# Kernel tuning notes

Hardware: AMD Instinct MI355X
Metric: run time of the kernel (lower is better)

Reference implementation:

```python
import jax, jax.numpy as jnp
import numpy as np
import math

B, T, HID = 2, 2048, 2048
NH, KH, HD = 32, 8, 64
G = NH // KH  # query heads per kv head
EPS = 1e-6
BASE = 10000.0


def _rope_sin_cos(t_len):
    inv_freq = 1.0 / (BASE ** (jnp.arange(0, HD, 2, dtype=jnp.float32) / HD))  # [HD/2]
    t = jnp.arange(t_len, dtype=jnp.float32)
    freqs = t[:, None] * inv_freq[None, :]  # [T, HD/2]
    return jnp.sin(freqs), jnp.cos(freqs)


def _apply_rope(x, sin, cos):
    # x: [B,H,T,D], pairwise interleaved rotation
    b, h, t, d = x.shape
    xr = x.reshape(b, h, t, d // 2, 2)
    x1, x2 = xr[..., 0], xr[..., 1]
    rot1 = x1 * cos - x2 * sin
    rot2 = x1 * sin + x2 * cos
    return jnp.stack((rot1, rot2), axis=-1).reshape(b, h, t, d)


def _rmsnorm(x, w):
    var = jnp.mean(x * x, axis=-1, keepdims=True)
    return x * jax.lax.rsqrt(var + EPS) * w


def setup_inputs() -> dict:
    key = jax.random.key(0)
    ks = jax.random.split(key, 5)
    s = 0.02
    return {
        "hidden_states": jax.random.normal(ks[0], (B, T, HID), jnp.float32),
        "wq": jax.random.normal(ks[1], (HID, HID), jnp.float32) * s,
        "wk": jax.random.normal(ks[2], (HID, KH * HD), jnp.float32) * s,
        "wv": jax.random.normal(ks[3], (HID, KH * HD), jnp.float32) * s,
        "wo": jax.random.normal(ks[4], (HID, HID), jnp.float32) * s,
        "q_norm_w": jnp.ones((HD,), jnp.float32),
        "k_norm_w": jnp.ones((HD,), jnp.float32),
    }


def reference(hidden_states, wq, wk, wv, wo, q_norm_w, k_norm_w):
    b, t, _ = hidden_states.shape
    # fused-ish QKV projections
    q = (hidden_states @ wq).reshape(b, t, NH, HD).transpose(0, 2, 1, 3)   # [B,NH,T,D]
    k = (hidden_states @ wk).reshape(b, t, KH, HD).transpose(0, 2, 1, 3)   # [B,KH,T,D]
    v = (hidden_states @ wv).reshape(b, t, KH, HD).transpose(0, 2, 1, 3)   # [B,KH,T,D]

    sin, cos = _rope_sin_cos(t)  # [T, D/2]
    q = _rmsnorm(_apply_rope(q, sin, cos), q_norm_w)
    k = _rmsnorm(_apply_rope(k, sin, cos), k_norm_w)

    scale = 1.0 / math.sqrt(HD)
    # grouped attention without materializing repeated KV
    qg = q.reshape(b, KH, G, t, HD)
    scores = jnp.einsum('bkgqd,bkld->bkgql', qg, k) * scale  # [B,KH,G,Tq,Tk]

    qi = jax.lax.broadcasted_iota(jnp.int32, (t, t), 0)
    ki = jax.lax.broadcasted_iota(jnp.int32, (t, t), 1)
    causal = ki <= qi
    scores = jnp.where(causal, scores, jnp.float32(-jnp.inf))

    attn = jax.nn.softmax(scores, axis=-1)
    ctx = jnp.einsum('bkgql,bkld->bkgqd', attn, v)  # [B,KH,G,T,D]
    ctx = ctx.reshape(b, NH, t, HD).transpose(0, 2, 1, 3).reshape(b, t, NH * HD)
    return ctx @ wo
```

## Files before the change

### kernel.cpp

```cpp
#include <hip/hip_runtime.h>
#include <math.h>
#include <stdint.h>

#define B_   2
#define T_   2048
#define HID_ 2048
#define NH_  32
#define KH_  8
#define HD_  64
#define LDQKV 3072

typedef unsigned short u16;
typedef __attribute__((ext_vector_type(8))) short v8s;
typedef __attribute__((ext_vector_type(4))) float v4f;

__device__ inline v4f mfma16(v8s a, v8s b, v4f c) {
    return __builtin_amdgcn_mfma_f32_16x16x32_bf16(a, b, c, 0, 0, 0);
}
__device__ inline u16 f2bf(float f) {
    uint32_t u = __float_as_uint(f);
    u += 0x7fff + ((u >> 16) & 1);
    return (u16)(u >> 16);
}
__device__ inline float bf2f(u16 h) { return __uint_as_float(((uint32_t)h) << 16); }
__device__ inline uint32_t cvtpk_bf16(float lo, float hi) {
    uint32_t r;
    asm("v_cvt_pk_bf16_f32 %0, %1, %2" : "=v"(r) : "v"(lo), "v"(hi));
    return r;
}

#define GLDS(g, s)                                                                     \
    __builtin_amdgcn_global_load_lds(                                                  \
        (const __attribute__((address_space(1))) uint32_t*)(uintptr_t)(g),             \
        (__attribute__((address_space(3))) uint32_t*)(uint32_t)(uintptr_t)(s), 16, 0, 0)

__global__ __launch_bounds__(256) void conv_f32_bf16(const float* __restrict__ in,
                                                     u16* __restrict__ out, int n4) {
    int i = blockIdx.x * 256 + threadIdx.x;
    if (i >= n4) return;
    float4 v = ((const float4*)in)[i];
    ushort4 o = {f2bf(v.x), f2bf(v.y), f2bf(v.z), f2bf(v.w)};
    ((ushort4*)out)[i] = o;
}

__global__ __launch_bounds__(256) void trconv4(const float* __restrict__ s0,
                                               const float* __restrict__ s1,
                                               const float* __restrict__ s2,
                                               const float* __restrict__ s3,
                                               u16* __restrict__ d0, u16* __restrict__ d1,
                                               u16* __restrict__ d2, u16* __restrict__ d3) {
    const int z = blockIdx.z;
    const float* in = (z == 0) ? s0 : (z == 1) ? s1 : (z == 2) ? s2 : s3;
    u16* out = (z == 0) ? d0 : (z == 1) ? d1 : (z == 2) ? d2 : d3;
    const int R = 2048;
    const int C = (z == 1 || z == 2) ? 512 : 2048;
    const int r0 = blockIdx.y * 64, c0 = blockIdx.x * 64;
    if (c0 >= C) return;

    __shared__ float t[64][65];
    const int tid = threadIdx.x;
#pragma unroll
    for (int i = 0; i < 16; ++i) {
        int idx = i * 256 + tid, r = idx >> 6, c = idx & 63;
        t[r][c] = in[(size_t)(r0 + r) * C + c0 + c];
    }
    __syncthreads();
#pragma unroll
    for (int i = 0; i < 16; ++i) {
        int idx = i * 256 + tid, r = idx >> 6, c = idx & 63;
        out[(size_t)(c0 + r) * R + r0 + c] = f2bf(t[c][r]);
    }
}

__global__ __launch_bounds__(256) void rope_table(float2* __restrict__ tab) {
    int i = blockIdx.x * 256 + threadIdx.x;
    int t = i >> 5, p = i & 31;
    float fr = (float)t * exp2f((float)p * (-13.28771237954945f / 32.0f));
    float2 sc; sc.x = sinf(fr); sc.y = cosf(fr);
    tab[i] = sc;
}

__global__ __launch_bounds__(256) void vtrans(const u16* __restrict__ V, u16* __restrict__ Vt) {
    const int t0 = blockIdx.x * 64, kh = blockIdx.y, b = blockIdx.z;
    const int tid = threadIdx.x;
    __shared__ __align__(16) u16 tl[64][72];
#pragma unroll
    for (int p = 0; p < 2; ++p) {
        int c = p * 256 + tid, trow = c >> 3, d8 = (c & 7) * 8;
        *(v8s*)&tl[trow][d8] =
            *(const v8s*)(V + (size_t)(b * T_ + t0 + trow) * LDQKV + kh * HD_ + d8);
    }
    __syncthreads();
#pragma unroll
    for (int p = 0; p < 2; ++p) {
        int c = p * 256 + tid, drow = c >> 3, t8 = (c & 7) * 8;
        v8s o;
#pragma unroll
        for (int j = 0; j < 8; ++j) o[j] = (short)tl[t8 + j][drow];
        *(v8s*)(Vt + ((size_t)((b * KH_ + kh) * HD_) + drow) * T_ + t0 + t8) = o;
    }
}

template <bool OBF>
__global__ __launch_bounds__(256) void gemm_mfma(const u16* __restrict__ A,
                                                 const u16* __restrict__ Bt,
                                                 void* __restrict__ Cv,
                                                 int M, int N, int K) {
    __shared__ __align__(16) u16 Al[128 * 32];
    __shared__ __align__(16) u16 Bl[128 * 32];
    const int tid = threadIdx.x;
    const int l = tid & 63;
    const int wid = tid >> 6;
    const int wr = wid >> 1, wc = wid & 1;
    const int lr = l & 15, lg = l >> 4;

    const int nx = gridDim.x;
    const int nwg = nx * gridDim.y;
    const int id = blockIdx.y * nx + blockIdx.x;
    const int sw = (id & 7) * (nwg >> 3) + (id >> 3);
    const int row0 = (sw / nx) * 128, col0 = (sw % nx) * 128;

    v4f acc[4][4];
    const v4f Z4 = {0.f, 0.f, 0.f, 0.f};
#pragma unroll
    for (int i = 0; i < 4; ++i)
#pragma unroll
        for (int j = 0; j < 4; ++j) acc[i][j] = Z4;

    const int m0 = tid & 127;
    const int ch0 = tid >> 7, ch1 = (256 + tid) >> 7;
    const u16* ga0 = A + (size_t)(row0 + m0) * K + ch0 * 8;
    const u16* ga1 = A + (size_t)(row0 + m0) * K + ch1 * 8;
    const u16* gb0 = Bt + (size_t)(col0 + m0) * K + ch0 * 8;
    const u16* gb1 = Bt + (size_t)(col0 + m0) * K + ch1 * 8;
    const int wbase = __builtin_amdgcn_readfirstlane(tid & 192);
    u16* la0 = &Al[wbase * 8];
    u16* la1 = &Al[(256 + wbase) * 8];
    u16* lb0 = &Bl[wbase * 8];
    u16* lb1 = &Bl[(256 + wbase) * 8];

    for (int k0 = 0; k0 < K; k0 += 32) {
        __syncthreads();
        GLDS(ga0 + k0, la0);
        GLDS(ga1 + k0, la1);
        GLDS(gb0 + k0, lb0);
        GLDS(gb1 + k0, lb1);
        __syncthreads();
        v8s af[4], bfr[4];
#pragma unroll
        for (int i = 0; i < 4; ++i) {
            af[i]  = *(const v8s*)&Al[(lg * 128 + wr * 64 + i * 16 + lr) * 8];
            bfr[i] = *(const v8s*)&Bl[(lg * 128 + wc * 64 + i * 16 + lr) * 8];
        }
#pragma unroll
        for (int i = 0; i < 4; ++i)
#pragma unroll
            for (int j = 0; j < 4; ++j) acc[i][j] = mfma16(af[i], bfr[j], acc[i][j]);
    }

#pragma unroll
    for (int i = 0; i < 4; ++i)
#pragma unroll
        for (int j = 0; j < 4; ++j)
#pragma unroll
            for (int r = 0; r < 4; ++r) {
                int row = row0 + wr * 64 + i * 16 + lg * 4 + r;
                int col = col0 + wc * 64 + j * 16 + lr;
                float v = acc[i][j][r];
                if (OBF) ((u16*)Cv)[(size_t)row * N + col] = f2bf(v);
                else     ((float*)Cv)[(size_t)row * N + col] = v;
            }
}

__global__ __launch_bounds__(256) void rope_rms2(u16* __restrict__ X,
                                                 const float* __restrict__ qw,
                                                 const float* __restrict__ kw,
                                                 const float2* __restrict__ tab) {
    int pair = blockIdx.x * 4 + (threadIdx.x >> 6);
    const int lane = threadIdx.x & 63;
    int row, h, off;
    const float* w;
    if (pair < 4096 * 32) { row = pair >> 5; h = pair & 31; off = 0; w = qw; }
    else { pair -= 4096 * 32; row = pair >> 3; h = pair & 7; off = 2048; w = kw; }
    const int t = row & (T_ - 1);

    u16* px = X + (size_t)row * LDQKV + off + h * HD_ + lane;
    float x = bf2f(*px);
    float2 sc = tab[t * 32 + (lane >> 1)];
    float other = __shfl_xor(x, 1, 64);
    float r = (lane & 1) ? fmaf(other, sc.x, x * sc.y) : fmaf(x, sc.y, -(other * sc.x));
    float sq = r * r;
#pragma unroll
    for (int offv = 32; offv >= 1; offv >>= 1) sq += __shfl_xor(sq, offv, 64);
    float invn = rsqrtf(sq * (1.0f / 64.0f) + 1e-6f);
    *px = f2bf(r * invn * w[lane]);
}

__global__ __launch_bounds__(512, 2) void attn_mfma(const u16* __restrict__ Qb,
                                                    const u16* __restrict__ Kb,
                                                    const u16* __restrict__ VTb,
                                                    u16* __restrict__ Ctx) {
    const int qt = gridDim.x - 1 - blockIdx.x;
    const int kh = blockIdx.y, b = blockIdx.z;
    const int tid = threadIdx.x, w = tid >> 6, l = tid & 63;
    const int lr = l & 15, lg = l >> 4;

    __shared__ __align__(16) u16 Kbuf[2][128 * 64];
    __shared__ __align__(16) u16 Vbuf[2][64 * 128];
    __shared__ __align__(16) uint32_t Ps[8][16][68];

    v8s qf[4][2];
#pragma unroll
    for (int g = 0; g < 4; ++g) {
        const u16* qp = Qb + (size_t)(b * T_ + qt * 128 + w * 16 + lr) * LDQKV +
                        (kh * 4 + g) * HD_ + lg * 8;
        qf[g][0] = *(const v8s*)qp;
        qf[g][1] = *(const v8s*)(qp + 32);
    }

    const int u0 = tid, u1 = 512 + tid;
    const int kr0 = u0 >> 3, kc0 = (u0 & 7) ^ (kr0 & 7);
    const int kr1 = u1 >> 3, kc1 = (u1 & 7) ^ (kr1 & 7);
    const u16* kg0 = Kb + (size_t)(b * T_ + kr0) * LDQKV + kh * HD_ + kc0 * 8;
    const u16* kg1 = Kb + (size_t)(b * T_ + kr1) * LDQKV + kh * HD_ + kc1 * 8;
    const int vr0 = u0 >> 4, vc0 = (u0 & 15) ^ (vr0 & 15);
    const int vr1 = u1 >> 4, vc1 = (u1 & 15) ^ (vr1 & 15);
    const u16* vg0 = VTb + ((size_t)((b * KH_ + kh) * HD_) + vr0) * T_ + vc0 * 8;
    const u16* vg1 = VTb + ((size_t)((b * KH_ + kh) * HD_) + vr1) * T_ + vc1 * 8;
    const int wu64 = __builtin_amdgcn_readfirstlane(w * 64);

    const v4f Z4 = {0.f, 0.f, 0.f, 0.f};
    v4f o[4][4];
    float lsum[4];
#pragma unroll
    for (int g = 0; g < 4; ++g) {
        lsum[g] = 0.f;
#pragma unroll
        for (int d = 0; d < 4; ++d) o[g][d] = Z4;
    }

    auto stage = [&](int bufi, int kt) {
        const size_t ko = (size_t)kt * 128 * LDQKV;
        const int vo = kt * 128;
        GLDS(kg0 + ko, &Kbuf[bufi][wu64 * 8]);
        GLDS(kg1 + ko, &Kbuf[bufi][(512 + wu64) * 8]);
        GLDS(vg0 + vo, &Vbuf[bufi][wu64 * 8]);
        GLDS(vg1 + vo, &Vbuf[bufi][(512 + wu64) * 8]);
    };

    const float C1 = 0.18033688011112042f;
    const float C0 = -11.541560327111707f;
    const int swz8 = lr & 7;

    auto body = [&](const u16* Kc, const u16* Vc, bool masked) {
#pragma unroll
        for (int g = 0; g < 4; ++g) {
            v4f s[8];
#pragma unroll
            for (int j = 0; j < 8; ++j) s[j] = Z4;
#pragma unroll
            for (int ks = 0; ks < 2; ++ks) {
#pragma unroll
                for (int j = 0; j < 8; ++j)
                    s[j] = mfma16(*(const v8s*)&Kc[(j * 16 + lr) * 64 + (((ks * 4 + lg) ^ swz8) * 8)],
                                  qf[g][ks], s[j]);
            }
#pragma unroll
            for (int j = 0; j < 8; ++j) {
                float p[4];
#pragma unroll
                for (int r = 0; r < 4; ++r) {
                    float pv = exp2f(fmaf(s[j][r], C1, C0));
                    if (masked && (j * 16 + lg * 4 + r) > (w * 16 + lr)) pv = 0.f;
                    p[r] = pv;
                }
                lsum[g] += (p[0] + p[1]) + (p[2] + p[3]);
                Ps[w][lr][j * 8 + lg * 2 + 0] = cvtpk_bf16(p[0], p[1]);
                Ps[w][lr][j * 8 + lg * 2 + 1] = cvtpk_bf16(p[2], p[3]);
            }
            asm volatile("s_waitcnt lgkmcnt(0)" ::: "memory");
#pragma unroll
            for (int ks = 0; ks < 4; ++ks) {
                v8s pf = *(const v8s*)&Ps[w][lr][ks * 16 + lg * 4];
#pragma unroll
                for (int dj = 0; dj < 4; ++dj)
                    o[g][dj] = mfma16(*(const v8s*)&Vc[(dj * 16 + lr) * 128 + (((ks * 4 + lg) ^ lr) * 8)],
                                      pf, o[g][dj]);
            }
        }
    };

    stage(0, 0);
    int buf = 0;
    for (int kt = 0; kt < qt; ++kt) {
        stage(buf ^ 1, kt + 1);
        asm volatile("s_waitcnt vmcnt(4)" ::: "memory");
        __builtin_amdgcn_s_barrier();
        body(Kbuf[buf], Vbuf[buf], false);
        asm volatile("s_waitcnt lgkmcnt(0)" ::: "memory");
        __builtin_amdgcn_s_barrier();
        buf ^= 1;
    }
    asm volatile("s_waitcnt vmcnt(0)" ::: "memory");
    __builtin_amdgcn_s_barrier();
    body(Kbuf[buf], Vbuf[buf], true);

#pragma unroll
    for (int g = 0; g < 4; ++g) {
        float t1 = lsum[g] + __shfl_xor(lsum[g], 16, 64);
        float inv = 1.0f / (t1 + __shfl_xor(t1, 32, 64));
        u16* cp = Ctx + (size_t)(b * T_ + qt * 128 + w * 16 + lr) * (NH_ * HD_) +
                  (kh * 4 + g) * HD_ + lg * 4;
#pragma unroll
        for (int dj = 0; dj < 4; ++dj) {
            ushort4 ov = {f2bf(o[g][dj][0] * inv), f2bf(o[g][dj][1] * inv),
                          f2bf(o[g][dj][2] * inv), f2bf(o[g][dj][3] * inv)};
            *(ushort4*)(cp + dj * 16) = ov;
        }
    }
}

extern "C" void kernel_launch(void* const* d_in, const int* in_sizes, int n_in,
                              void* d_out, int out_size, void* d_ws, size_t ws_size,
                              hipStream_t stream) {
    const float* hs  = (const float*)d_in[0];
    const float* wq  = (const float*)d_in[1];
    const float* wk  = (const float*)d_in[2];
    const float* wv  = (const float*)d_in[3];
    const float* wo  = (const float*)d_in[4];
    const float* qnw = (const float*)d_in[5];
    const float* knw = (const float*)d_in[6];
    float* out = (float*)d_out;
    (void)in_sizes; (void)n_in; (void)out_size; (void)ws_size;

    char* p = (char*)d_ws;
    auto alloc = [&](size_t bytes) { void* r = (void*)p; p += (bytes + 255) & ~(size_t)255; return r; };
    u16* hsb   = (u16*)alloc((size_t)4096 * 2048 * 2);
    u16* wqkvt = (u16*)alloc((size_t)3072 * 2048 * 2);
    u16* qkvb  = (u16*)alloc((size_t)4096 * 3072 * 2);
    u16* wot   = (u16*)alloc((size_t)2048 * 2048 * 2);
    u16* ctx   = (u16*)alloc((size_t)4096 * 2048 * 2);
    u16* vt    = (u16*)alloc((size_t)B_ * KH_ * HD_ * T_ * 2);
    float2* tab = (float2*)alloc((size_t)T_ * 32 * sizeof(float2));

    conv_f32_bf16<<<(4096 * 2048 / 4 + 255) / 256, 256, 0, stream>>>(hs, hsb, 4096 * 2048 / 4);
    trconv4<<<dim3(32, 32, 4), 256, 0, stream>>>(wq, wk, wv, wo,
                                                 wqkvt,
                                                 wqkvt + (size_t)2048 * 2048,
                                                 wqkvt + (size_t)2560 * 2048,
                                                 wot);
    rope_table<<<(T_ * 32) / 256, 256, 0, stream>>>(tab);

    gemm_mfma<true><<<dim3(3072 / 128, 4096 / 128), 256, 0, stream>>>(hsb, wqkvt, qkvb, 4096, 3072, 2048);

    rope_rms2<<<(4096 * 40) / 4, 256, 0, stream>>>(qkvb, qnw, knw, tab);
    vtrans<<<dim3(T_ / 64, KH_, B_), 256, 0, stream>>>(qkvb + 2560, vt);

    attn_mfma<<<dim3(T_ / 128, KH_, B_), 512, 0, stream>>>(qkvb, qkvb + 2048, vt, ctx);

    gemm_mfma<false><<<dim3(2048 / 128, 4096 / 128), 256, 0, stream>>>(ctx, wot, out, 4096, 2048, 2048);
}
```

Baseline: 440.7 us.

## Replace GEMM with double-buffered 256-row tile kernel using swizzled LDS and ping-pong

Replaces the simple single-buffered 128x128 MFMA GEMM with a 512-thread kernel that uses 256xBN tiles, a K-step of 64 split into two halves, and double-buffered LDS. Global-to-LDS loads for later tiles are issued while MFMAs on the current tile run, with explicit vmcnt waits, barriers and setprio to interleave memory and compute. LDS addresses are XOR-swizzled to avoid bank conflicts. It uses larger register and LDS footprints and hand-placed waitcnt counts, and it is applied to both the QKV and output projections.

```diff
diff --git a/kernel.cpp b/kernel.cpp
--- a/kernel.cpp
+++ b/kernel.cpp
@@ -33,6 +33,10 @@
     __builtin_amdgcn_global_load_lds(                                                  \
         (const __attribute__((address_space(1))) uint32_t*)(uintptr_t)(g),             \
         (__attribute__((address_space(3))) uint32_t*)(uint32_t)(uintptr_t)(s), 16, 0, 0)
+
+#define BAR() __builtin_amdgcn_s_barrier()
+#define LG0() asm volatile("s_waitcnt lgkmcnt(0)" ::: "memory")
+#define VMW(n) asm volatile("s_waitcnt vmcnt(" #n ")" ::: "memory")
 
 __global__ __launch_bounds__(256) void conv_f32_bf16(const float* __restrict__ in,
                                                      u16* __restrict__ out, int n4) {
@@ -101,75 +105,129 @@
     }
 }
 
-template <bool OBF>
-__global__ __launch_bounds__(256) void gemm_mfma(const u16* __restrict__ A,
-                                                 const u16* __restrict__ Bt,
-                                                 void* __restrict__ Cv,
-                                                 int M, int N, int K) {
-    __shared__ __align__(16) u16 Al[128 * 32];
-    __shared__ __align__(16) u16 Bl[128 * 32];
+template <int BN, bool OBF>
+__global__ __launch_bounds__(512, 2) void gemm8(const u16* __restrict__ A,
+                                                const u16* __restrict__ Bt,
+                                                void* __restrict__ Cv,
+                                                int M, int N, int K) {
+    constexpr int NW_N = BN / 64;
+    constexpr int MF = (NW_N == 4) ? 8 : 4;
+    constexpr int MH = MF / 2;
+
+    __shared__ __align__(16) u16 Al[2][2][8192];
+    __shared__ __align__(16) u16 Bl[2][2][BN * 32];
+
     const int tid = threadIdx.x;
-    const int l = tid & 63;
-    const int wid = tid >> 6;
-    const int wr = wid >> 1, wc = wid & 1;
+    const int w = tid >> 6, l = tid & 63;
     const int lr = l & 15, lg = l >> 4;
+    const int warp_m = w / NW_N, warp_n = w % NW_N;
 
     const int nx = gridDim.x;
     const int nwg = nx * gridDim.y;
     const int id = blockIdx.y * nx + blockIdx.x;
     const int sw = (id & 7) * (nwg >> 3) + (id >> 3);
-    const int row0 = (sw / nx) * 128, col0 = (sw % nx) * 128;
-
-    v4f acc[4][4];
+    const int row0 = (sw / nx) * 256, col0 = (sw % nx) * BN;
+
+    const int NT = K >> 6;
+
+    const int srow = tid >> 2;
+    const int sg = (tid & 3) ^ ((tid >> 3) & 3);
+    const u16* aS = A + (size_t)(row0 + srow) * K + sg * 8;
+    const u16* bS = Bt + (size_t)(col0 + srow) * K + sg * 8;
+    const int wbase = __builtin_amdgcn_readfirstlane(w) * 512;
+
+    const int aoff = ((warp_m * (MF * 16) + lr) * 4 + (lg ^ ((lr >> 1) & 3))) * 8;
+    const int boff = ((warp_n * 64 + lr) * 4 + (lg ^ ((lr >> 1) & 3))) * 8;
+
+#define SA(b_, kh_, tau_)                                                              \
+    {                                                                                  \
+        GLDS(aS + (tau_) * 64 + (kh_) * 32, &Al[b_][kh_][wbase]);                      \
+        GLDS(aS + (size_t)128 * K + (tau_) * 64 + (kh_) * 32, &Al[b_][kh_][4096 + wbase]); \
+    }
+#define SB(b_, kh_, tau_)                                                              \
+    {                                                                                  \
+        GLDS(bS + (tau_) * 64 + (kh_) * 32, &Bl[b_][kh_][wbase]);                      \
+        if constexpr (BN == 256)                                                       \
+            GLDS(bS + (size_t)128 * K + (tau_) * 64 + (kh_) * 32, &Bl[b_][kh_][4096 + wbase]); \
+    }
+#define LDB(U)                                                                         \
+    _Pragma("unroll") for (int j = 0; j < 4; ++j)                                      \
+        bf[j] = *(const v8s*)((U) + boff + j * 512);
+#define LDA(U, mh)                                                                     \
+    _Pragma("unroll") for (int fi = 0; fi < MH; ++fi)                                  \
+        af[fi] = *(const v8s*)((U) + aoff + ((mh) * MH + fi) * 512);
+#define MM(mh)                                                                         \
+    _Pragma("unroll") for (int fi = 0; fi < MH; ++fi)                                  \
+        _Pragma("unroll") for (int j = 0; j < 4; ++j)                                  \
+            acc[(mh) * MH + fi][j] = mfma16(af[fi], bf[j], acc[(mh) * MH + fi][j]);
+
+    v4f acc[MF][4];
     const v4f Z4 = {0.f, 0.f, 0.f, 0.f};
 #pragma unroll
-    for (int i = 0; i < 4; ++i)
+    for (int i = 0; i < MF; ++i)
 #pragma unroll
         for (int j = 0; j < 4; ++j) acc[i][j] = Z4;
 
-    const int m0 = tid & 127;
-    const int ch0 = tid >> 7, ch1 = (256 + tid) >> 7;
-    const u16* ga0 = A + (size_t)(row0 + m0) * K + ch0 * 8;
-    const u16* ga1 = A + (size_t)(row0 + m0) * K + ch1 * 8;
-    const u16* gb0 = Bt + (size_t)(col0 + m0) * K + ch0 * 8;
-    const u16* gb1 = Bt + (size_t)(col0 + m0) * K + ch1 * 8;
-    const int wbase = __builtin_amdgcn_readfirstlane(tid & 192);
-    u16* la0 = &Al[wbase * 8];
-    u16* la1 = &Al[(256 + wbase) * 8];
-    u16* lb0 = &Bl[wbase * 8];
-    u16* lb1 = &Bl[(256 + wbase) * 8];
-
-    for (int k0 = 0; k0 < K; k0 += 32) {
-        __syncthreads();
-        GLDS(ga0 + k0, la0);
-        GLDS(ga1 + k0, la1);
-        GLDS(gb0 + k0, lb0);
-        GLDS(gb1 + k0, lb1);
-        __syncthreads();
-        v8s af[4], bfr[4];
-#pragma unroll
-        for (int i = 0; i < 4; ++i) {
-            af[i]  = *(const v8s*)&Al[(lg * 128 + wr * 64 + i * 16 + lr) * 8];
-            bfr[i] = *(const v8s*)&Bl[(lg * 128 + wc * 64 + i * 16 + lr) * 8];
-        }
-#pragma unroll
-        for (int i = 0; i < 4; ++i)
-#pragma unroll
-            for (int j = 0; j < 4; ++j) acc[i][j] = mfma16(af[i], bfr[j], acc[i][j]);
-    }
-
-#pragma unroll
-    for (int i = 0; i < 4; ++i)
+    SA(0, 0, 0); SB(0, 0, 0); SA(0, 1, 0); SB(0, 1, 0); SA(1, 0, 1); SB(1, 0, 1);
+    if constexpr (BN == 256) { VMW(8); } else { VMW(6); }
+    BAR();
+
+    int buf = 0;
+    for (int tau = 0; tau < NT; ++tau) {
+        const u16* A0 = &Al[buf][0][0];
+        const u16* A1 = &Al[buf][1][0];
+        const u16* B0 = &Bl[buf][0][0];
+        const u16* B1 = &Bl[buf][1][0];
+        const int nb = buf ^ 1;
+        const bool s1 = (tau + 1 < NT), s2 = (tau + 2 < NT);
+        v8s af[MH], bf[4];
+
+        LDB(B0); LDA(A0, 0);
+        if (s1) SA(nb, 1, tau + 1);
+        BAR();
+        __builtin_amdgcn_s_setprio(1); MM(0); __builtin_amdgcn_s_setprio(0);
+        BAR();
+        LDA(A0, 1);
+        if (s1) SB(nb, 1, tau + 1);
+        BAR();
+        __builtin_amdgcn_s_setprio(1); MM(1); __builtin_amdgcn_s_setprio(0);
+        LG0();
+        if (s1) { if constexpr (BN == 256) { VMW(8); } else { VMW(6); } }
+        else    { VMW(0); }
+        BAR();
+        LDB(B1); LDA(A1, 0);
+        if (s2) SA(buf, 0, tau + 2);
+        BAR();
+        __builtin_amdgcn_s_setprio(1); MM(0); __builtin_amdgcn_s_setprio(0);
+        BAR();
+        LDA(A1, 1);
+        if (s2) SB(buf, 0, tau + 2);
+        BAR();
+        __builtin_amdgcn_s_setprio(1); MM(1); __builtin_amdgcn_s_setprio(0);
+        LG0();
+        if (s2)      { if constexpr (BN == 256) { VMW(8); } else { VMW(6); } }
+        else if (s1) { if constexpr (BN == 256) { VMW(4); } else { VMW(3); } }
+        BAR();
+        buf ^= 1;
+    }
+
+#pragma unroll
+    for (int fi = 0; fi < MF; ++fi)
 #pragma unroll
         for (int j = 0; j < 4; ++j)
 #pragma unroll
             for (int r = 0; r < 4; ++r) {
-                int row = row0 + wr * 64 + i * 16 + lg * 4 + r;
-                int col = col0 + wc * 64 + j * 16 + lr;
-                float v = acc[i][j][r];
+                int row = row0 + warp_m * (MF * 16) + fi * 16 + lg * 4 + r;
+                int col = col0 + warp_n * 64 + j * 16 + lr;
+                float v = acc[fi][j][r];
                 if (OBF) ((u16*)Cv)[(size_t)row * N + col] = f2bf(v);
                 else     ((float*)Cv)[(size_t)row * N + col] = v;
             }
+#undef SA
+#undef SB
+#undef LDA
+#undef LDB
+#undef MM
 }
 
 __global__ __launch_bounds__(256) void rope_rms2(u16* __restrict__ X,
@@ -351,12 +409,12 @@
                                                  wot);
     rope_table<<<(T_ * 32) / 256, 256, 0, stream>>>(tab);
 
-    gemm_mfma<true><<<dim3(3072 / 128, 4096 / 128), 256, 0, stream>>>(hsb, wqkvt, qkvb, 4096, 3072, 2048);
+    gemm8<256, true><<<dim3(3072 / 256, 4096 / 256), 512, 0, stream>>>(hsb, wqkvt, qkvb, 4096, 3072, 2048);
 
     rope_rms2<<<(4096 * 40) / 4, 256, 0, stream>>>(qkvb, qnw, knw, tab);
     vtrans<<<dim3(T_ / 64, KH_, B_), 256, 0, stream>>>(qkvb + 2560, vt);
 
     attn_mfma<<<dim3(T_ / 128, KH_, B_), 512, 0, stream>>>(qkvb, qkvb + 2048, vt, ctx);
 
-    gemm_mfma<false><<<dim3(2048 / 128, 4096 / 128), 256, 0, stream>>>(ctx, wot, out, 4096, 2048, 2048);
-}
+    gemm8<128, false><<<dim3(2048 / 128, 4096 / 256), 512, 0, stream>>>(ctx, wot, out, 4096, 2048, 2048);
+}
```

New measurement: 358.3 us. -18.7%, faster.
